# Kernel tuning notes

Hardware: AMD Instinct MI355X
Metric: run time of the kernel (lower is better)

Reference implementation:

```python
import jax, jax.numpy as jnp
import numpy as np
from jax.scipy.special import xlogy

B, N, F_IN, D, L = 32, 512, 20, 128, 5
NEG = -1e7


def setup_inputs() -> dict:
    key = jax.random.key(0)
    ks = jax.random.split(key, 24)
    s = lambda n: 1.0 / np.sqrt(n)
    inp = {}
    inp["fatoms"] = jax.random.normal(ks[0], (B, N, F_IN), jnp.float32)
    # normalized dense multi-relation adjacency (row sums ~1 for stability)
    inp["adj"] = jax.random.uniform(ks[1], (B, N, N, 3), jnp.float32) * (2.0 / N)
    inp["all_mask"] = jnp.ones((B, N, 1), jnp.float32)
    inp["current_mask"] = jnp.ones((B, N, 1), jnp.float32)
    inp["prob_mask"] = jnp.ones((B, N, 1), jnp.float32)
    inp["focus"] = jax.random.randint(ks[2], (B, 1), 0, N)
    inp["action_batch"] = jax.random.randint(ks[3], (B, 3), 0, 2)
    # embeddings (bias-free Linear(20, D))
    inp["W_emb"] = jax.random.normal(ks[4], (F_IN, D)) * s(F_IN)
    inp["W_cemb"] = jax.random.normal(ks[5], (F_IN, D)) * s(F_IN)
    # per-iteration, per-relation GCN weights [L,3,D,D] and biases [L,3,D]
    inp["actor_W"] = jax.random.normal(ks[6], (L, 3, D, D)) * s(D)
    inp["actor_b"] = jnp.zeros((L, 3, D), jnp.float32)
    inp["critic_W"] = jax.random.normal(ks[7], (L, 3, D, D)) * s(D)
    inp["critic_b"] = jnp.zeros((L, 3, D), jnp.float32)
    # end_selection_layer: Linear(2D,D)+ReLU+Linear(D,1,no bias)
    inp["We1"] = jax.random.normal(ks[8], (2 * D, D)) * s(2 * D)
    inp["be1"] = jnp.zeros((D,), jnp.float32)
    inp["We2"] = jax.random.normal(ks[9], (D, 1)) * s(D)
    # bond_selection_layer: Linear(2D,D)+ReLU+Linear(D,3,no bias)+Softmax
    inp["Wb1"] = jax.random.normal(ks[10], (2 * D, D)) * s(2 * D)
    inp["bb1"] = jnp.zeros((D,), jnp.float32)
    inp["Wb2"] = jax.random.normal(ks[11], (D, 3)) * s(D)
    # stop_selection_layer: Linear(D,D)+ReLU+Linear(D,2,no bias)+Softmax
    inp["Ws1"] = jax.random.normal(ks[12], (D, D)) * s(D)
    inp["bs1"] = jnp.zeros((D,), jnp.float32)
    inp["Ws2"] = jax.random.normal(ks[13], (D, 2)) * s(D)
    # qlayer: Linear(2D,D)+ReLU+Linear(D,1)
    inp["Wq1"] = jax.random.normal(ks[14], (2 * D, D)) * s(2 * D)
    inp["bq1"] = jnp.zeros((D,), jnp.float32)
    inp["Wq2"] = jax.random.normal(ks[15], (D, 1)) * s(D)
    inp["bq2"] = jnp.zeros((1,), jnp.float32)
    return inp


def _entropy(p):
    return -jnp.sum(xlogy(p, p), axis=-1)


def reference(fatoms, adj, all_mask, current_mask, prob_mask, focus, action_batch,
              W_emb, W_cemb, actor_W, actor_b, critic_W, critic_b,
              We1, be1, We2, Wb1, bb1, Wb2, Ws1, bs1, Ws2, Wq1, bq1, Wq2, bq2):
    def gcn_stack(x, Ws_all, bs_all):
        def step(h, wb):
            W, b = wb  # [3,D,D], [3,D]
            hw = jnp.einsum('bmd,rde->rbme', h, W) + b[:, None, None, :]
            msg = jax.nn.relu(jnp.einsum('bnmr,rbme->rbne', adj, hw))
            return jnp.sum(msg, axis=0) * all_mask, None
        h, _ = jax.lax.scan(step, x, (Ws_all, bs_all))
        return h

    # actor and critic feature updates
    x_a = gcn_stack(jax.nn.relu(fatoms @ W_emb), actor_W, actor_b)   # [B,N,D]
    x_c = gcn_stack(jax.nn.relu(fatoms @ W_cemb), critic_W, critic_b)

    # maxpool_sumpool + qlayer
    max_mask = jnp.where(current_mask == 1.0, 0.0, NEG)
    sum_pool = jnp.sum(x_c * current_mask, axis=1)                   # [B,D]
    max_pool = jnp.max(x_c + max_mask, axis=1)                       # [B,D]
    q_in = jnp.concatenate([sum_pool, max_pool], axis=-1)            # [B,2D]
    qvalue = jax.nn.relu(q_in @ Wq1 + bq1) @ Wq2 + bq2               # [B,1]

    pm = jnp.where(prob_mask == 1.0, 0.0, NEG)                       # [B,N,1]
    b, n, d = x_a.shape
    start = jnp.take_along_axis(x_a, jnp.broadcast_to(focus[:, :, None], (b, 1, d)), axis=1)  # [B,1,D]

    end_input = jnp.concatenate([jnp.broadcast_to(start, (b, n, d)), x_a], axis=-1)           # [B,N,2D]
    logits = jax.nn.relu(end_input @ We1 + be1) @ We2 + pm           # [B,N,1]
    end_probs = jax.nn.softmax(logits, axis=1)[..., 0]               # [B,N]

    end_idx = action_batch[:, 0:1]
    end_atom = jnp.take_along_axis(x_a, jnp.broadcast_to(end_idx[:, :, None], (b, 1, d)), axis=1)
    end_prob_new = jnp.take_along_axis(end_probs, end_idx, axis=1)   # [B,1]

    bond_in = jnp.concatenate([start, end_atom], axis=-1)[:, 0, :]   # [B,2D]
    bond_probs = jax.nn.softmax(jax.nn.relu(bond_in @ Wb1 + bb1) @ Wb2, axis=-1)  # [B,3]
    bond_prob_new = jnp.take_along_axis(bond_probs, action_batch[:, 1:2], axis=1)

    stop_probs = jax.nn.softmax(jax.nn.relu(start[:, 0, :] @ Ws1 + bs1) @ Ws2, axis=-1)  # [B,2]
    stop_prob_new = jnp.take_along_axis(stop_probs, action_batch[:, 2:3], axis=1)

    prob_batch_new = jnp.concatenate([end_prob_new, bond_prob_new, stop_prob_new], axis=-1)  # [B,3]
    entropy = _entropy(end_probs) + _entropy(bond_probs) + _entropy(stop_probs)             # [B]
    return prob_batch_new, entropy, qvalue
```

## Files before the change

kernel.cpp:

```cpp
#include <hip/hip_runtime.h>
#include <cstdint>
#include <cstddef>

typedef unsigned short u16;
typedef __bf16 bfx8 __attribute__((ext_vector_type(8)));
typedef float f32x4 __attribute__((ext_vector_type(4)));

#define NEGV -10000000.0f
constexpr int cB = 32, cN = 512, cD = 128, cF = 20, cL = 5;

__device__ __forceinline__ float bf2f(u16 h){ unsigned u = ((unsigned)h)<<16; return __builtin_bit_cast(float,u); }
__device__ __forceinline__ u16 f2bf(float f){ unsigned u = __builtin_bit_cast(unsigned,f); return (u16)((u + 0x7fffu + ((u>>16)&1u))>>16); }

constexpr int WOF_EMB  = 0;
constexpr int WOF_CEMB = 2560;
constexpr int WOF_AW   = 5120;
constexpr int WOF_CW   = 250880;
constexpr int WOF_WE1  = 496640;
constexpr int WOF_WE2  = 529408;
constexpr int WOF_WB1  = 529536;
constexpr int WOF_WB2  = 562304;
constexpr int WOF_WS1  = 562688;
constexpr int WOF_WS2  = 579072;
constexpr int WOF_WQ1  = 579328;
constexpr int WOF_WQ2  = 612096;
constexpr int WTOTAL   = 612224;

struct WPtrs { const void* p[12]; };

__global__ __launch_bounds__(256) void canon_w(WPtrs wp, u16* __restrict__ Wc){
  __shared__ int s_flag;
  int t = threadIdx.x;
  if (t == 0) s_flag = 0;
  __syncthreads();
  const u16* probe = (const u16*)wp.p[2];
  int big = 0;
  #pragma unroll
  for (int i=0;i<2;++i){
    float a = fabsf(bf2f(probe[i*256 + t]));
    if (!(a < 1e10f)) big = 1;
  }
  if (__any(big)) s_flag = 1;
  __syncthreads();
  int flag = s_flag;
  int i = blockIdx.x*256 + t;
  if (i >= WTOTAL) return;
  constexpr int offs[13] = {WOF_EMB, WOF_CEMB, WOF_AW, WOF_CW, WOF_WE1, WOF_WE2,
                            WOF_WB1, WOF_WB2, WOF_WS1, WOF_WS2, WOF_WQ1, WOF_WQ2, WTOTAL};
  int a = 0;
  #pragma unroll
  for (int k = 1; k < 12; ++k) if (i >= offs[k]) a = k;
  int off = i - offs[a];
  const void* p = wp.p[a];
  Wc[i] = flag ? f2bf(((const float*)p)[off]) : ((const u16*)p)[off];
}

__global__ __launch_bounds__(256) void prep_w(const u16* __restrict__ Wc, u16* __restrict__ WT){
  __shared__ u16 sh[128*129];
  int blk = blockIdx.x;
  const u16* in;
  if (blk < 30){
    int s = blk/15; int lr = blk%15;
    in = Wc + (s ? WOF_CW : WOF_AW) + (size_t)lr*16384;
  } else {
    in = Wc + WOF_WE1 + 128*cD;
  }
  u16* out = WT + (size_t)blk*16384;
  int t = threadIdx.x;
  #pragma unroll 4
  for (int i=0;i<64;++i){ int idx=i*256+t; int d=idx>>7, e=idx&127; sh[e*129+d]=in[idx]; }
  __syncthreads();
  #pragma unroll 4
  for (int i=0;i<64;++i){ int idx=i*256+t; int e=idx>>7, d=idx&127; out[idx]=sh[e*129+d]; }
}

__global__ __launch_bounds__(128) void emb(const float* __restrict__ fatoms, const u16* __restrict__ Wc, u16* __restrict__ h0){
  int row = blockIdx.x;
  int s = row >> 14; int bn = row & 16383;
  __shared__ float fa[cF];
  int t = threadIdx.x;
  if (t < cF) fa[t] = fatoms[(size_t)bn*cF + t];
  __syncthreads();
  const u16* W = Wc + (s ? WOF_CEMB : WOF_EMB);
  float acc = 0.f;
  #pragma unroll
  for (int f=0; f<cF; ++f) acc += fa[f]*bf2f(W[f*cD + t]);
  h0[((size_t)s*cB*cN + bn)*cD + t] = f2bf(fmaxf(acc,0.f));
}

__device__ __forceinline__ void stage16k(const u16* gbase, int ldaB, int ktB, char* sm, int w, int l){
  #pragma unroll
  for (int i=0;i<4;++i){
    int c = (w<<2) + i;
    int row = (c<<3) + (l>>3);
    const char* src = (const char*)gbase + (size_t)row*ldaB + ktB + (((l&7)^(row&7))<<4);
    __builtin_amdgcn_global_load_lds((const __attribute__((address_space(1))) void*)src,
                                     (__attribute__((address_space(3))) void*)(sm + (c<<10)), 16, 0, 0);
  }
}
__device__ __forceinline__ void stage8k(const u16* gbase, int ldaB, int ktB, char* sm, int w, int l){
  #pragma unroll
  for (int i=0;i<2;++i){
    int c = (w<<1) + i;
    int row = (c<<3) + (l>>3);
    const char* src = (const char*)gbase + (size_t)row*ldaB + ktB + (((l&7)^(row&7))<<4);
    __builtin_amdgcn_global_load_lds((const __attribute__((address_space(1))) void*)src,
                                     (__attribute__((address_space(3))) void*)(sm + (c<<10)), 16, 0, 0);
  }
}
__device__ __forceinline__ bfx8 readfrag(const char* sm, int row, int kk, int l){
  int col = ((kk<<6) + ((l>>4)<<4)) ^ ((row&7)<<4);
  return *(const bfx8*)(sm + row*128 + col);
}
template<int MF,int NF>
__device__ __forceinline__ void mfma_tile(const char* A, const char* Bm, int ra, int rb, int l, f32x4 (&acc)[MF][NF]){
  #pragma unroll
  for (int kk=0; kk<2; ++kk){
    bfx8 af[MF], bv[NF];
    #pragma unroll
    for (int f=0; f<MF; ++f) af[f] = readfrag(A,  ra+(f<<4)+(l&15), kk, l);
    #pragma unroll
    for (int f=0; f<NF; ++f) bv[f] = readfrag(Bm, rb+(f<<4)+(l&15), kk, l);
    #pragma unroll
    for (int mf=0; mf<MF; ++mf)
      #pragma unroll
      for (int nf=0; nf<NF; ++nf)
        acc[mf][nf] = __builtin_amdgcn_mfma_f32_16x16x32_bf16(af[mf], bv[nf], acc[mf][nf], 0,0,0);
  }
}
__device__ __forceinline__ void flush16k(const char* P, char* gbase, int ldB, int colB, int t){
  #pragma unroll
  for (int j=0;j<4;++j){
    int p = j*4096 + t*16;
    int e = p>>7, col = p&127;
    int4 v = *(const int4*)(P + p);
    *(int4*)(gbase + (size_t)e*ldB + colB + col) = v;
  }
}

__global__ __launch_bounds__(256,2) void k1_hw(const u16* __restrict__ WT, const u16* __restrict__ h,
                                               const float* __restrict__ actor_b, const float* __restrict__ critic_b,
                                               u16* __restrict__ hwT, int layer){
  __shared__ __align__(16) char smA[16384];
  __shared__ __align__(16) char smB[16384];
  int blk = blockIdx.x;
  int nt = blk & 3; int srb = blk >> 2;
  int s = srb/96; int rb = srb%96; int r = rb>>5; int b = rb&31;
  int t = threadIdx.x, w = t>>6, l = t&63, wr = w>>1, wc = w&1;
  const u16* Abase = WT + (size_t)(s*15 + layer*3 + r)*16384;
  const u16* Bbase = h + ((size_t)s*cB*cN + (size_t)b*cN + (size_t)nt*128)*cD;
  f32x4 acc[4][4];
  #pragma unroll
  for (int i=0;i<4;++i){ acc[i][0]=f32x4{0,0,0,0}; acc[i][1]=f32x4{0,0,0,0}; acc[i][2]=f32x4{0,0,0,0}; acc[i][3]=f32x4{0,0,0,0}; }
  for (int kt=0; kt<2; ++kt){
    __syncthreads();
    stage16k(Abase, 256, kt*128, smA, w, l);
    stage16k(Bbase, 256, kt*128, smB, w, l);
    __syncthreads();
    mfma_tile<4,4>(smA, smB, wr<<6, wc<<6, l, acc);
  }
  const float* bias = (s ? critic_b : actor_b) + (layer*3 + r)*cD;
  __syncthreads();
  char* OPh = wc ? smB : smA;
  #pragma unroll
  for (int mf=0; mf<4; ++mf)
    #pragma unroll
    for (int nf=0; nf<4; ++nf)
      #pragma unroll
      for (int j=0; j<4; ++j){
        int e  = (wr<<6) + (mf<<4) + ((l>>4)<<2) + j;
        int mh = (nf<<4) + (l&15);
        *(u16*)(OPh + e*128 + mh*2) = f2bf(acc[mf][nf][j] + bias[e]);
      }
  __syncthreads();
  char* outB = (char*)(hwT + (size_t)((s*3+r)*cB + b)*cD*cN);
  flush16k(smA, outB, 1024, nt*256 + 0,   t);
  flush16k(smB, outB, 1024, nt*256 + 128, t);
}

template<int L0>
__global__ __launch_bounds__(256,2) void k2f(const float* __restrict__ adj, u16* __restrict__ adjT,
                                             const u16* __restrict__ hwT_in, u16* __restrict__ hwT_out,
                                             const float* __restrict__ all_mask, const u16* __restrict__ WT,
                                             const float* __restrict__ actor_b, const float* __restrict__ critic_b,
                                             u16* __restrict__ hfin, int layer){
  __shared__ __align__(16) char pool[73728];
  int blk = blockIdx.x;
  int xcd = blk & 7; int slot = blk >> 3;
  int b = (slot>>4)*8 + xcd;
  int rest = slot & 15; int s = rest>>3; int mt = rest&7;
  int t = threadIdx.x, w = t>>6, l = t&63, wr = w>>1, wc = w&1;
  const u16* hwB = hwT_in + (size_t)(s*3*cB + b)*cD*cN;
  const size_t hwRs = (size_t)cB*cD*cN;
  f32x4 sum[2][4];
  #pragma unroll
  for (int i=0;i<2;++i)
    #pragma unroll
    for (int j=0;j<4;++j) sum[i][j]=f32x4{0,0,0,0};

  if constexpr (L0){
    f32x4 a3[3][2][4];
    #pragma unroll
    for (int r=0;r<3;++r)
      #pragma unroll
      for (int i=0;i<2;++i)
        #pragma unroll
        for (int j=0;j<4;++j) a3[r][i][j]=f32x4{0,0,0,0};
    const int nl  = t>>2;
    const int m8  = (t&3)*2;
    const float* asrc = adj + ((size_t)(b*cN + mt*64 + nl)*cN + m8*8)*3;
    for (int kt=0; kt<8; ++kt){
      stage16k(hwB,        1024, kt*128, pool+24576, w, l);
      stage16k(hwB+hwRs,   1024, kt*128, pool+40960, w, l);
      stage16k(hwB+2*hwRs, 1024, kt*128, pool+57344, w, l);
      float4 v[12];
      const float* sp = asrc + (size_t)kt*64*3;
      #pragma unroll
      for (int q=0;q<12;++q) v[q] = ((const float4*)sp)[q];
      __syncthreads();
      const float* vf = (const float*)v;
      #pragma unroll
      for (int i=0;i<2;++i){
        int m8i = m8 + i;
        #pragma unroll
        for (int r=0;r<3;++r){
          __align__(16) u16 o[8];
          #pragma unroll
          for (int k=0;k<8;++k) o[k] = f2bf(vf[i*24 + k*3 + r]);
          *(int4*)(pool + r*8192 + nl*128 + ((m8i*16) ^ ((nl&7)<<4))) = *(const int4*)o;
          if (s == 0)
            *(int4*)(adjT + ((size_t)(r*cB + b)*cN + mt*64 + nl)*cN + kt*64 + m8i*8) = *(const int4*)o;
        }
      }
      __syncthreads();
      #pragma unroll
      for (int r=0;r<3;++r)
        mfma_tile<2,4>(pool + r*8192, pool + 24576 + r*16384, wr<<5, wc<<6, l, a3[r]);
    }
    #pragma unroll
    for (int r=0;r<3;++r)
      #pragma unroll
      for (int mf=0;mf<2;++mf)
        #pragma unroll
        for (int nf=0;nf<4;++nf)
          #pragma unroll
          for (int j=0;j<4;++j)
            sum[mf][nf][j] += fmaxf(a3[r][mf][nf][j], 0.f);
  } else {
    const u16* adjB = adjT + ((size_t)b*cN + (size_t)mt*64)*cN;
    const size_t adjRs = (size_t)cB*cN*cN;
    for (int r=0;r<3;++r){
      f32x4 acc[2][4];
      #pragma unroll
      for (int i=0;i<2;++i)
        #pragma unroll
        for (int j=0;j<4;++j) acc[i][j]=f32x4{0,0,0,0};
      for (int kt=0;kt<8;++kt){
        __syncthreads();
        stage8k (adjB + (size_t)r*adjRs, 1024, kt*128, pool, w, l);
        stage16k(hwB  + (size_t)r*hwRs,  1024, kt*128, pool+8192, w, l);
        __syncthreads();
        mfma_tile<2,4>(pool, pool+8192, wr<<5, wc<<6, l, acc);
      }
      #pragma unroll
      for (int mf=0;mf<2;++mf)
        #pragma unroll
        for (int nf=0;nf<4;++nf)
          #pragma unroll
          for (int j=0;j<4;++j)
            sum[mf][nf][j] += fmaxf(acc[mf][nf][j], 0.f);
    }
  }
  __syncthreads();
  char* hT0 = pool + (L0 ? 0 : 24576);
  char* hT1 = hT0 + 8192;
  char* OP  = pool + (L0 ? 57344 : 0);
  #pragma unroll
  for (int mf=0; mf<2; ++mf)
    #pragma unroll
    for (int nf=0; nf<4; ++nf)
      #pragma unroll
      for (int j=0; j<4; ++j){
        int nloc = (wr<<5) + (mf<<4) + ((l>>4)<<2) + j;
        int e    = (wc<<6) + (nf<<4) + (l&15);
        int n    = mt*64 + nloc;
        u16 hv = f2bf(sum[mf][nf][j] * all_mask[b*cN + n]);
        char* base = (e & 64) ? hT1 : hT0;
        *(u16*)(base + nloc*128 + (((e&63)*2) ^ ((nloc&7)<<4))) = hv;
      }
  if (layer == cL-1){
    __syncthreads();
    char* gdst = (char*)(hfin + ((size_t)(s*cB + b)*cN + (size_t)mt*64)*cD);
    #pragma unroll
    for (int j=0;j<4;++j){
      int p = j*4096 + t*16;
      int nloc = p>>8, ebyte = p&255;
      char* hbase = (ebyte & 128) ? hT1 : hT0;
      int chunk = ebyte & 127;
      int4 v = *(const int4*)(hbase + nloc*128 + (chunk ^ ((nloc&7)<<4)));
      *(int4*)(gdst + (size_t)nloc*256 + ebyte) = v;
    }
    return;
  }
  char* W0 = pool + (L0 ? 24576 : 40960);
  char* W1 = W0 + 16384;
  for (int r=0; r<3; ++r){
    __syncthreads();
    const u16* Wbase = WT + (size_t)(s*15 + (layer+1)*3 + r)*16384;
    stage16k(Wbase, 256, 0,   W0, w, l);
    stage16k(Wbase, 256, 128, W1, w, l);
    __syncthreads();
    f32x4 acc2[4][2];
    #pragma unroll
    for (int i=0;i<4;++i){ acc2[i][0]=f32x4{0,0,0,0}; acc2[i][1]=f32x4{0,0,0,0}; }
    mfma_tile<4,2>(W0, hT0, wr<<6, wc<<5, l, acc2);
    mfma_tile<4,2>(W1, hT1, wr<<6, wc<<5, l, acc2);
    const float* bias = (s ? critic_b : actor_b) + ((layer+1)*3 + r)*cD;
    #pragma unroll
    for (int mf=0; mf<4; ++mf)
      #pragma unroll
      for (int nf=0; nf<2; ++nf)
        #pragma unroll
        for (int j=0; j<4; ++j){
          int e   = (wr<<6) + (mf<<4) + ((l>>4)<<2) + j;
          int m64 = (wc<<5) + (nf<<4) + (l&15);
          *(u16*)(OP + e*128 + m64*2) = f2bf(acc2[mf][nf][j] + bias[e]);
        }
    __syncthreads();
    char* outB = (char*)(hwT_out + (size_t)((s*3+r)*cB + b)*cD*cN);
    flush16k(OP, outB, 1024, mt*128, t);
  }
}

__global__ __launch_bounds__(256) void pool_part(const u16* __restrict__ xc, const float* __restrict__ cmask,
                                                 float* __restrict__ part){
  int blk = blockIdx.x;
  int b = blk >> 4, c = blk & 15;
  int t = threadIdx.x; int d = t & 127, nh = t >> 7;
  const u16* x = xc + ((size_t)b*cN + c*32 + nh*16)*cD;
  const float* cm = cmask + (size_t)b*cN + c*32 + nh*16;
  float sm = 0.f, mx = -3e38f;
  #pragma unroll
  for (int i=0;i<16;++i){
    float v = bf2f(x[(size_t)i*cD + d]);
    float m = cm[i];
    sm += v*m;
    mx = fmaxf(mx, v + (m==1.0f ? 0.f : NEGV));
  }
  __shared__ float s_sm[2][128], s_mx[2][128];
  s_sm[nh][d] = sm; s_mx[nh][d] = mx;
  __syncthreads();
  if (nh == 0){
    float* dst = part + ((size_t)b*16 + c)*256;
    dst[d]       = sm + s_sm[1][d];
    dst[128 + d] = fmaxf(mx, s_mx[1][d]);
  }
}

__global__ __launch_bounds__(256,2) void end_logits2(const u16* __restrict__ xa, const u16* __restrict__ WT,
                                                     const u16* __restrict__ Wc, const int* __restrict__ focus,
                                                     const float* __restrict__ be1,
                                                     const float* __restrict__ prob_mask, float* __restrict__ logits){
  __shared__ __align__(16) char smA[16384];
  __shared__ __align__(16) char smB[16384];
  __shared__ float s_start[128], sh_sc[128], sh_w2[128], rowsum[2][128];
  int blk = blockIdx.x;
  int nt = blk & 3, b = blk >> 2;
  int t = threadIdx.x, w = t>>6, l = t&63, wr = w>>1, wc = w&1;
  if (t < 128){
    s_start[t] = bf2f(xa[((size_t)b*cN + focus[b])*cD + t]);
    sh_w2[t]   = bf2f(Wc[WOF_WE2 + t]);
  }
  __syncthreads();
  if (t < 128){
    float a = be1[t];
    #pragma unroll 4
    for (int k=0;k<128;++k) a += s_start[k]*bf2f(Wc[WOF_WE1 + k*cD + t]);
    sh_sc[t] = a;
  }
  const u16* Abase = xa + ((size_t)b*cN + (size_t)nt*128)*cD;
  const u16* Bbase = WT + (size_t)30*16384;
  f32x4 acc[4][4];
  #pragma unroll
  for (int i=0;i<4;++i){ acc[i][0]=f32x4{0,0,0,0}; acc[i][1]=f32x4{0,0,0,0}; acc[i][2]=f32x4{0,0,0,0}; acc[i][3]=f32x4{0,0,0,0}; }
  for (int kt=0; kt<2; ++kt){
    __syncthreads();
    stage16k(Abase, 256, kt*128, smA, w, l);
    stage16k(Bbase, 256, kt*128, smB, w, l);
    __syncthreads();
    mfma_tile<4,4>(smA, smB, wr<<6, wc<<6, l, acc);
  }
  float p[4][4];
  #pragma unroll
  for (int mf=0;mf<4;++mf)
    #pragma unroll
    for (int j=0;j<4;++j) p[mf][j] = 0.f;
  #pragma unroll
  for (int mf=0; mf<4; ++mf)
    #pragma unroll
    for (int nf=0; nf<4; ++nf){
      int e = (wc<<6) + (nf<<4) + (l&15);
      float scv = sh_sc[e], w2 = sh_w2[e];
      #pragma unroll
      for (int j=0; j<4; ++j)
        p[mf][j] += fmaxf(acc[mf][nf][j] + scv, 0.f) * w2;
    }
  #pragma unroll
  for (int mf=0; mf<4; ++mf)
    #pragma unroll
    for (int j=0; j<4; ++j){
      float v = p[mf][j];
      #pragma unroll
      for (int o=1;o<16;o<<=1) v += __shfl_xor(v, o, 64);
      if ((l&15)==0) rowsum[wc][(wr<<6) + (mf<<4) + ((l>>4)<<2) + j] = v;
    }
  __syncthreads();
  if (t < 128){
    int n = nt*128 + t;
    float pm = (prob_mask[b*cN + n]==1.0f) ? 0.f : NEGV;
    logits[b*cN + n] = rowsum[0][t] + rowsum[1][t] + pm;
  }
}

__global__ __launch_bounds__(128) void heads_final(const float* __restrict__ part, const u16* __restrict__ Wc,
                                                   const float* __restrict__ bq1, const float* __restrict__ bq2,
                                                   const float* __restrict__ logits, const int* __restrict__ action,
                                                   const u16* __restrict__ xa, const int* __restrict__ focus,
                                                   const float* __restrict__ bb1, const float* __restrict__ bs1,
                                                   float* __restrict__ out){
  int b = blockIdx.x, t = threadIdx.x;
  __shared__ float qin[256];
  __shared__ float sv[128], ev[128];
  __shared__ float redq[2], red5[5][2];
  __shared__ float HendSh;
  sv[t] = bf2f(xa[((size_t)b*cN + focus[b])*cD + t]);
  ev[t] = bf2f(xa[((size_t)b*cN + action[b*3])*cD + t]);
  float sm = 0.f, mx = -3e38f;
  #pragma unroll
  for (int c=0;c<16;++c){
    const float* src = part + ((size_t)b*16 + c)*256;
    sm += src[t];
    mx = fmaxf(mx, src[128 + t]);
  }
  qin[t] = sm; qin[128+t] = mx;
  __syncthreads();
  float acc = bq1[t];
  #pragma unroll 4
  for (int k=0; k<256; ++k) acc += qin[k]*bf2f(Wc[WOF_WQ1 + k*cD + t]);
  float hc = fmaxf(acc,0.f)*bf2f(Wc[WOF_WQ2 + t]);
  #pragma unroll
  for (int o=32;o>0;o>>=1) hc += __shfl_down(hc, o, 64);
  if ((t&63)==0) redq[t>>6] = hc;
  if (t < 64){
    float v[8];
    #pragma unroll
    for (int i=0;i<8;++i) v[i] = logits[b*cN + i*64 + t];
    float m = v[0];
    #pragma unroll
    for (int i=1;i<8;++i) m = fmaxf(m, v[i]);
    #pragma unroll
    for (int o=32;o>0;o>>=1) m = fmaxf(m, __shfl_xor(m, o, 64));
    float e[8]; float s = 0.f;
    #pragma unroll
    for (int i=0;i<8;++i){ e[i] = expf(v[i]-m); s += e[i]; }
    #pragma unroll
    for (int o=32;o>0;o>>=1) s += __shfl_xor(s, o, 64);
    float lns = logf(s);
    float pl = 0.f;
    #pragma unroll
    for (int i=0;i<8;++i){ float p = e[i]/s; pl += p*((v[i]-m) - lns); }
    #pragma unroll
    for (int o=32;o>0;o>>=1) pl += __shfl_xor(pl, o, 64);
    int idx = action[b*3 + 0];
    if (t == (idx & 63)){
      float pe = 0.f;
      #pragma unroll
      for (int i=0;i<8;++i) if ((idx>>6)==i) pe = e[i];
      out[b*3 + 0] = pe / s;
    }
    if (t == 0) HendSh = -pl;
  }
  __syncthreads();
  float ab = bb1[t], as_ = bs1[t];
  #pragma unroll 4
  for (int k=0;k<128;++k){ float svk = sv[k]; ab += svk*bf2f(Wc[WOF_WB1 + k*cD + t]); as_ += svk*bf2f(Wc[WOF_WS1 + k*cD + t]); }
  #pragma unroll 4
  for (int k=0;k<128;++k) ab += ev[k]*bf2f(Wc[WOF_WB1 + (128+k)*cD + t]);
  float hb = fmaxf(ab,0.f), hs = fmaxf(as_,0.f);
  float r0 = hb*bf2f(Wc[WOF_WB2 + t*3+0]);
  float r1 = hb*bf2f(Wc[WOF_WB2 + t*3+1]);
  float r2 = hb*bf2f(Wc[WOF_WB2 + t*3+2]);
  float r3 = hs*bf2f(Wc[WOF_WS2 + t*2+0]);
  float r4 = hs*bf2f(Wc[WOF_WS2 + t*2+1]);
  #pragma unroll
  for (int o=32;o>0;o>>=1){
    r0 += __shfl_xor(r0,o,64); r1 += __shfl_xor(r1,o,64); r2 += __shfl_xor(r2,o,64);
    r3 += __shfl_xor(r3,o,64); r4 += __shfl_xor(r4,o,64);
  }
  if ((t&63)==0){ int wid=t>>6; red5[0][wid]=r0; red5[1][wid]=r1; red5[2][wid]=r2; red5[3][wid]=r3; red5[4][wid]=r4; }
  __syncthreads();
  if (t==0){
    out[128 + b] = redq[0] + redq[1] + bq2[0];
    auto xlx = [](float p){ return p > 0.f ? p*logf(p) : 0.f; };
    float bl0=red5[0][0]+red5[0][1], bl1=red5[1][0]+red5[1][1], bl2=red5[2][0]+red5[2][1];
    float sl0=red5[3][0]+red5[3][1], sl1=red5[4][0]+red5[4][1];
    float m = fmaxf(fmaxf(bl0,bl1),bl2);
    float e0=expf(bl0-m), e1=expf(bl1-m), e2=expf(bl2-m); float S=e0+e1+e2;
    float p0=e0/S, p1=e1/S, p2=e2/S;
    float Hb = -(xlx(p0) + xlx(p1) + xlx(p2));
    int a1 = action[b*3+1];
    out[b*3+1] = (a1==0)?p0:((a1==1)?p1:p2);
    float ms = fmaxf(sl0,sl1);
    float f0=expf(sl0-ms), f1=expf(sl1-ms); float T=f0+f1;
    float q0=f0/T, q1=f1/T;
    float Hs = -(xlx(q0) + xlx(q1));
    int a2 = action[b*3+2];
    out[b*3+2] = (a2==0)?q0:q1;
    out[96+b] = HendSh + Hb + Hs;
  }
}

extern "C" void kernel_launch(void* const* d_in, const int* in_sizes, int n_in,
                              void* d_out, int out_size, void* d_ws, size_t ws_size,
                              hipStream_t stream){
  const float* fatoms      = (const float*)d_in[0];
  const float* adj         = (const float*)d_in[1];
  const float* all_mask    = (const float*)d_in[2];
  const float* current_mask= (const float*)d_in[3];
  const float* prob_mask   = (const float*)d_in[4];
  const int*   focus       = (const int*)d_in[5];
  const int*   action      = (const int*)d_in[6];
  const float* actor_b     = (const float*)d_in[10];
  const float* critic_b    = (const float*)d_in[12];
  const float* be1         = (const float*)d_in[14];
  const float* bb1         = (const float*)d_in[17];
  const float* bs1         = (const float*)d_in[20];
  const float* bq1         = (const float*)d_in[23];
  const float* bq2         = (const float*)d_in[25];

  char* ws = (char*)d_ws;
  size_t o = 0;
  u16* adjT = (u16*)(ws + o);  o += (size_t)3*cB*cN*cN*2;
  u16* WT   = (u16*)(ws + o);  o += (size_t)31*16384*2;
  u16* hbuf = (u16*)(ws + o);  o += (size_t)2*2*cB*cN*cD*2;
  u16* hwT0 = (u16*)(ws + o);  o += (size_t)2*3*cB*cD*cN*2;
  u16* hwT1 = (u16*)(ws + o);  o += (size_t)2*3*cB*cD*cN*2;
  u16* Wcan = (u16*)(ws + o);  o += (size_t)WTOTAL*2;
  float* part   = (float*)(ws + o); o += (size_t)cB*16*256*4;
  float* logits = (float*)(ws + o); o += (size_t)cB*cN*4;
  float* out = (float*)d_out;

  WPtrs wp;
  wp.p[0]=d_in[7];  wp.p[1]=d_in[8];  wp.p[2]=d_in[9];  wp.p[3]=d_in[11];
  wp.p[4]=d_in[13]; wp.p[5]=d_in[15]; wp.p[6]=d_in[16]; wp.p[7]=d_in[18];
  wp.p[8]=d_in[19]; wp.p[9]=d_in[21]; wp.p[10]=d_in[22]; wp.p[11]=d_in[24];

  canon_w<<<dim3((WTOTAL+255)/256), dim3(256), 0, stream>>>(wp, Wcan);
  prep_w<<<dim3(31), dim3(256), 0, stream>>>(Wcan, WT);
  emb<<<dim3(2*cB*cN), dim3(128), 0, stream>>>(fatoms, Wcan, hbuf);

  const size_t hstride = (size_t)2*cB*cN*cD;
  u16* hfin = hbuf + hstride;
  k1_hw<<<dim3(768), dim3(256), 0, stream>>>(WT, hbuf, actor_b, critic_b, hwT0, 0);
  k2f<1><<<dim3(512), dim3(256), 0, stream>>>(adj, adjT, hwT0, hwT1, all_mask, WT, actor_b, critic_b, hfin, 0);
  for (int l=1; l<cL; ++l){
    u16* win  = (l&1) ? hwT1 : hwT0;
    u16* wout = (l&1) ? hwT0 : hwT1;
    k2f<0><<<dim3(512), dim3(256), 0, stream>>>(adj, adjT, win, wout, all_mask, WT, actor_b, critic_b, hfin, l);
  }
  const u16* xa = hfin;
  const u16* xc = hfin + (size_t)cB*cN*cD;

  end_logits2<<<dim3(cB*4), dim3(256), 0, stream>>>(xa, WT, Wcan, focus, be1, prob_mask, logits);
  pool_part<<<dim3(cB*16), dim3(256), 0, stream>>>(xc, current_mask, part);
  heads_final<<<dim3(cB), dim3(128), 0, stream>>>(part, Wcan, bq1, bq2, logits, action, xa, focus, bb1, bs1, out);
}
```

Baseline: 257.1 us.

## Prefetch next adjacency tile and coalesce bf16 adjT stores via LDS

In the layer-0 path, the fp32 adjacency loads for the next k-tile are issued before the current tile's MFMAs, and explicit vmcnt waits with raw barriers replace __syncthreads, so global latency overlaps with compute. The transposed bf16 adjacency copy written to global memory is now read back from the swizzled LDS tile and stored in contiguous 16-byte chunks per row, instead of scattered per-thread writes. This adds register pressure from the double-buffered loads and relies on hand-tuned waitcnt values that must match the issued memory-op counts.

```diff
diff --git a/kernel.cpp b/kernel.cpp
--- a/kernel.cpp
+++ b/kernel.cpp
@@ -209,30 +209,56 @@
     const int nl  = t>>2;
     const int m8  = (t&3)*2;
     const float* asrc = adj + ((size_t)(b*cN + mt*64 + nl)*cN + m8*8)*3;
+    float4 v[12];
+    #pragma unroll
+    for (int q=0;q<12;++q) v[q] = ((const float4*)asrc)[q];
     for (int kt=0; kt<8; ++kt){
+      __builtin_amdgcn_s_barrier();
+      __builtin_amdgcn_sched_barrier(0);
       stage16k(hwB,        1024, kt*128, pool+24576, w, l);
       stage16k(hwB+hwRs,   1024, kt*128, pool+40960, w, l);
       stage16k(hwB+2*hwRs, 1024, kt*128, pool+57344, w, l);
-      float4 v[12];
-      const float* sp = asrc + (size_t)kt*64*3;
-      #pragma unroll
-      for (int q=0;q<12;++q) v[q] = ((const float4*)sp)[q];
-      __syncthreads();
+      __builtin_amdgcn_sched_barrier(0);
       const float* vf = (const float*)v;
+      __align__(16) u16 o[2][3][8];
+      #pragma unroll
+      for (int i=0;i<2;++i)
+        #pragma unroll
+        for (int r=0;r<3;++r)
+          #pragma unroll
+          for (int k=0;k<8;++k) o[i][r][k] = f2bf(vf[i*24 + k*3 + r]);
       #pragma unroll
       for (int i=0;i<2;++i){
         int m8i = m8 + i;
         #pragma unroll
+        for (int r=0;r<3;++r)
+          *(int4*)(pool + r*8192 + nl*128 + ((m8i*16) ^ ((nl&7)<<4))) = *(const int4*)&o[i][r][0];
+      }
+      if (kt < 7){
+        const float* sp = asrc + (size_t)(kt+1)*64*3;
+        #pragma unroll
+        for (int q=0;q<12;++q) v[q] = ((const float4*)sp)[q];
+      }
+      __builtin_amdgcn_sched_barrier(0);
+      if (kt < 7) asm volatile("s_waitcnt vmcnt(12)" ::: "memory");
+      else        asm volatile("s_waitcnt vmcnt(0)"  ::: "memory");
+      asm volatile("s_waitcnt lgkmcnt(0)" ::: "memory");
+      __builtin_amdgcn_sched_barrier(0);
+      __builtin_amdgcn_s_barrier();
+      __builtin_amdgcn_sched_barrier(0);
+      if (s == 0){
+        #pragma unroll
         for (int r=0;r<3;++r){
-          __align__(16) u16 o[8];
+          char* gb = (char*)adjT + (((size_t)(r*cB + b)*cN + (size_t)mt*64)*cN + (size_t)kt*64)*2;
           #pragma unroll
-          for (int k=0;k<8;++k) o[k] = f2bf(vf[i*24 + k*3 + r]);
-          *(int4*)(pool + r*8192 + nl*128 + ((m8i*16) ^ ((nl&7)<<4))) = *(const int4*)o;
-          if (s == 0)
-            *(int4*)(adjT + ((size_t)(r*cB + b)*cN + mt*64 + nl)*cN + kt*64 + m8i*8) = *(const int4*)o;
+          for (int j=0;j<2;++j){
+            int p = j*4096 + t*16;
+            int n2 = p>>7, chunk = p&127;
+            int4 val = *(const int4*)(pool + r*8192 + n2*128 + (chunk ^ ((n2&7)<<4)));
+            *(int4*)(gb + (size_t)n2*1024 + chunk) = val;
+          }
         }
       }
-      __syncthreads();
       #pragma unroll
       for (int r=0;r<3;++r)
         mfma_tile<2,4>(pool + r*8192, pool + 24576 + r*16384, wr<<5, wc<<6, l, a3[r]);
@@ -297,8 +323,8 @@
       int nloc = p>>8, ebyte = p&255;
       char* hbase = (ebyte & 128) ? hT1 : hT0;
       int chunk = ebyte & 127;
-      int4 v = *(const int4*)(hbase + nloc*128 + (chunk ^ ((nloc&7)<<4)));
-      *(int4*)(gdst + (size_t)nloc*256 + ebyte) = v;
+      int4 v2 = *(const int4*)(hbase + nloc*128 + (chunk ^ ((nloc&7)<<4)));
+      *(int4*)(gdst + (size_t)nloc*256 + ebyte) = v2;
     }
     return;
   }
```

Result: faster. 251.0 us (-2.4%).
